# Optimization experiments

Hardware: AMD Instinct MI355X
Metric: run time of the kernel (lower is better)

## Reference

```python
import jax, jax.numpy as jnp
import numpy as np

D = 1024
B, S = 4, 2048


def setup_inputs() -> dict:
    key = jax.random.key(0)
    ks = jax.random.split(key, 9)
    std = 1.0 / np.sqrt(D)
    x = jax.random.normal(ks[0], (B, S, D), dtype=jnp.float32)
    Wq = jax.random.normal(ks[1], (D, D), dtype=jnp.float32) * std
    bq = jax.random.normal(ks[2], (D,), dtype=jnp.float32) * std
    Wk = jax.random.normal(ks[3], (D, D), dtype=jnp.float32) * std
    bk = jax.random.normal(ks[4], (D,), dtype=jnp.float32) * std
    Wv = jax.random.normal(ks[5], (D, D), dtype=jnp.float32) * std
    bv = jax.random.normal(ks[6], (D,), dtype=jnp.float32) * std
    Wo = jax.random.normal(ks[7], (D, D), dtype=jnp.float32) * std
    bo = jax.random.normal(ks[8], (D,), dtype=jnp.float32) * std
    return {"x": x, "Wq": Wq, "bq": bq, "Wk": Wk, "bk": bk,
            "Wv": Wv, "bv": bv, "Wo": Wo, "bo": bo}


def reference(x, Wq, bq, Wk, bk, Wv, bv, Wo, bo):
    d = x.shape[-1]
    q = x @ Wq + bq          # [B, S, D]
    k = x @ Wk + bk          # [B, S, D] (first call: kv cache empty)
    v = x @ Wv + bv          # [B, S, D]
    scale = 1.0 / jnp.sqrt(jnp.asarray(d, dtype=x.dtype))
    att = jnp.einsum('bqd,bkd->bqk', q, k) * scale  # [B, S, S]
    sq, sk = q.shape[1], k.shape[1]
    causal = jnp.triu(jnp.ones((sq, sk), dtype=bool), k=1)
    att = jnp.where(causal, -jnp.inf, att)
    att = jax.nn.softmax(att, axis=-1)
    out = jnp.einsum('bqk,bkd->bqd', att, v)        # [B, S, D]
    return out @ Wo + bo
```

## Files before the change

kernel.cpp:

```cpp
#include <hip/hip_runtime.h>
#include <hip/hip_bf16.h>


typedef __attribute__((ext_vector_type(8))) __bf16 bf16x8;
typedef __attribute__((ext_vector_type(4))) float f32x4;
typedef __attribute__((ext_vector_type(8))) unsigned short u16x8;
typedef __attribute__((ext_vector_type(4))) float float4v;
typedef long long ll;

static __device__ __forceinline__ unsigned short f2b(float f) {
  unsigned int u = __float_as_uint(f);
  u += 0x7fffu + ((u >> 16) & 1u);
  return (unsigned short)(u >> 16);
}
static __device__ __forceinline__ float b2f(unsigned short b) {
  return __uint_as_float(((unsigned int)b) << 16);
}

static __device__ __forceinline__ void gload16(const unsigned short* g, unsigned short* l) {
  __builtin_amdgcn_global_load_lds(
      (const __attribute__((address_space(1))) void*)g,
      (__attribute__((address_space(3))) void*)l, 16, 0, 0);
}

__global__ __launch_bounds__(256) void cvt_f32_bf16(const float* __restrict__ in,
                                                    unsigned short* __restrict__ out,
                                                    long long n) {
  long long i = ((long long)blockIdx.x * 256 + threadIdx.x) * 8;
  if (i + 8 > n) return;
  float4v a = *(const float4v*)(in + i);
  float4v b = *(const float4v*)(in + i + 4);
  u16x8 o;
  o[0] = f2b(a[0]); o[1] = f2b(a[1]); o[2] = f2b(a[2]); o[3] = f2b(a[3]);
  o[4] = f2b(b[0]); o[5] = f2b(b[1]); o[6] = f2b(b[2]); o[7] = f2b(b[3]);
  *(u16x8*)(out + i) = o;
}

__global__ __launch_bounds__(256) void transpose_cvt(const float* __restrict__ in,
                                                     unsigned short* __restrict__ out, int n) {
  __shared__ float t[32][33];
  int bx = blockIdx.x * 32, by = blockIdx.y * 32;
  int tx = threadIdx.x, ty = threadIdx.y;
#pragma unroll
  for (int i = 0; i < 32; i += 8)
    t[ty + i][tx] = in[(ll)(by + ty + i) * n + bx + tx];
  __syncthreads();
#pragma unroll
  for (int i = 0; i < 32; i += 8)
    out[(ll)(bx + ty + i) * n + by + tx] = f2b(t[tx][ty + i]);
}

__global__ void concat2(const float* __restrict__ a, const float* __restrict__ b,
                        float* __restrict__ o, int n) {
  int i = blockIdx.x * 256 + threadIdx.x;
  if (i < n) { o[i] = a[i]; o[i + n] = b[i]; }
}

template <int CAUSAL>
__global__ __launch_bounds__(256, 2) void gemm_tn(
    const unsigned short* __restrict__ A, const unsigned short* __restrict__ B,
    const float* __restrict__ bias, void* __restrict__ C,
    int K, int lda, int ldb, int ldc,
    ll strideA, ll strideB, ll strideC,
    float alpha, int c_is_bf16, int bias_row) {
  __shared__ unsigned short sA[2][128][64];
  __shared__ unsigned short sB[2][128][64];

  const int tid = threadIdx.x;
  const int w = tid >> 6, lane = tid & 63;
  const int bz = blockIdx.z;
  const unsigned short* Ab = A + (ll)bz * strideA;
  const unsigned short* Bb = B + (ll)bz * strideB;
  const int brow = blockIdx.y * 128, bcol = blockIdx.x * 128;
  const int wr = (w >> 1) * 64, wc = (w & 1) * 64;
  const int lr = lane & 15, lk = lane >> 4;

  const int Keff = (CAUSAL == 2) ? (brow + 128) : K;
  const int nt = Keff >> 6;

  f32x4 acc[4][4];
#pragma unroll
  for (int i = 0; i < 4; ++i)
#pragma unroll
    for (int n = 0; n < 4; ++n) acc[i][n] = (f32x4){0.f, 0.f, 0.f, 0.f};

  auto STAGE = [&](int buf, int kb) {
#pragma unroll
    for (int it = 0; it < 4; ++it) {
      const int chunk = it * 4 + w;
      const int slot = chunk * 64 + lane;
      const int row = slot >> 3;
      const int kg = (slot & 7) ^ (row & 7);
      gload16(Ab + (ll)(brow + row) * lda + kb + kg * 8, &sA[buf][0][0] + chunk * 512);
      gload16(Bb + (ll)(bcol + row) * ldb + kb + kg * 8, &sB[buf][0][0] + chunk * 512);
    }
  };

  auto COMPUTE = [&](int buf) {
#pragma unroll
    for (int kk = 0; kk < 64; kk += 32) {
      bf16x8 af[4], bfr[4];
      const int kgb = (kk >> 3) + lk;
      const int sw = (kgb ^ (lr & 7)) * 8;
#pragma unroll
      for (int i = 0; i < 4; ++i) af[i] = *(const bf16x8*)&sA[buf][wr + i * 16 + lr][sw];
#pragma unroll
      for (int n = 0; n < 4; ++n) bfr[n] = *(const bf16x8*)&sB[buf][wc + n * 16 + lr][sw];
#pragma unroll
      for (int i = 0; i < 4; ++i)
#pragma unroll
        for (int n = 0; n < 4; ++n)
          acc[i][n] = __builtin_amdgcn_mfma_f32_16x16x32_bf16(af[i], bfr[n], acc[i][n], 0, 0, 0);
    }
  };

  STAGE(0, 0);
  __syncthreads();
  int cur = 0;
  for (int t = 0; t < nt - 1; ++t) {
    STAGE(cur ^ 1, (t + 1) << 6);
    COMPUTE(cur);
    __syncthreads();
    cur ^= 1;
  }
  COMPUTE(cur);

  ll cbase = (ll)bz * strideC;
#pragma unroll
  for (int i = 0; i < 4; ++i) {
    int row = brow + wr + i * 16 + lk * 4;
#pragma unroll
    for (int n = 0; n < 4; ++n) {
      int col = bcol + wc + n * 16 + lr;
#pragma unroll
      for (int r = 0; r < 4; ++r) {
        float bvv = bias ? (bias_row ? bias[row + r] : bias[col]) : 0.0f;
        float v = (acc[i][n][r] + bvv) * alpha;
        ll idx = cbase + (ll)(row + r) * ldc + col;
        if (c_is_bf16) ((unsigned short*)C)[idx] = f2b(v);
        else ((float*)C)[idx] = v;
      }
    }
  }
}

template <int CAUSAL>
__global__ __launch_bounds__(512, 2) void gemm8p(
    const unsigned short* __restrict__ A, const unsigned short* __restrict__ B,
    const float* __restrict__ bias, void* __restrict__ C,
    int K, int lda, int ldb, int ldc,
    ll strideA, ll strideB, ll strideC,
    float alpha, int c_is_bf16) {
  if (CAUSAL == 1 && blockIdx.x > blockIdx.y) return;

  __shared__ unsigned short smem[4 * 16384];

  const int tid = threadIdx.x;
  const int wid = tid >> 6, lane = tid & 63;
  const int wm = wid >> 2, wn = wid & 3;
  const int lr = lane & 15, lk = lane >> 4;
  const int bz = blockIdx.z;
  const unsigned short* Ab = A + (ll)bz * strideA;
  const unsigned short* Bb = B + (ll)bz * strideB;
  const int brow = blockIdx.y * 256, bcol = blockIdx.x * 256;
  const int nt = K >> 5;

  f32x4 acc[8][4];
#pragma unroll
  for (int m = 0; m < 8; ++m)
#pragma unroll
    for (int n = 0; n < 4; ++n) acc[m][n] = (f32x4){0.f, 0.f, 0.f, 0.f};

  auto STAGE_A = [&](int t) {
    unsigned short* lds = &smem[0] + (t & 3) * 16384;
    const int kb = t << 5;
#pragma unroll
    for (int h = 0; h < 2; ++h) {
      const int c = wid * 2 + h;
      const int row = c * 16 + (lane >> 2);
      const int kg = (lane & 3) ^ ((row >> 1) & 3);
      gload16(Ab + (ll)(brow + row) * lda + kb + kg * 8, lds + c * 512);
    }
  };
  auto STAGE_B = [&](int t) {
    unsigned short* lds = &smem[0] + (t & 3) * 16384 + 8192;
    const int kb = t << 5;
#pragma unroll
    for (int h = 0; h < 2; ++h) {
      const int c = wid * 2 + h;
      const int row = c * 16 + (lane >> 2);
      const int kg = (lane & 3) ^ ((row >> 1) & 3);
      gload16(Bb + (ll)(bcol + row) * ldb + kb + kg * 8, lds + c * 512);
    }
  };

  STAGE_A(0); STAGE_B(0);
  STAGE_A(1); STAGE_B(1);

  for (int t = 0; t < nt; ++t) {
    if (t < nt - 1) asm volatile("s_waitcnt vmcnt(4)" ::: "memory");
    else            asm volatile("s_waitcnt vmcnt(0)" ::: "memory");
    __builtin_amdgcn_s_barrier();

    const unsigned short* lds = &smem[0] + (t & 3) * 16384;
    bf16x8 bfrag[4], afrag[4];

#pragma unroll
    for (int n = 0; n < 4; ++n) {
      const int row = wn * 64 + n * 16 + lr;
      const int slot = lk ^ ((row >> 1) & 3);
      bfrag[n] = *(const bf16x8*)(lds + 8192 + row * 32 + slot * 8);
    }
#pragma unroll
    for (int m = 0; m < 4; ++m) {
      const int row = wm * 128 + m * 16 + lr;
      const int slot = lk ^ ((row >> 1) & 3);
      afrag[m] = *(const bf16x8*)(lds + row * 32 + slot * 8);
    }
    if (t + 2 < nt) STAGE_A(t + 2);
    __builtin_amdgcn_s_barrier();
    __builtin_amdgcn_s_setprio(1);
#pragma unroll
    for (int m = 0; m < 4; ++m)
#pragma unroll
      for (int n = 0; n < 4; ++n)
        acc[m][n] = __builtin_amdgcn_mfma_f32_16x16x32_bf16(afrag[m], bfrag[n], acc[m][n], 0, 0, 0);
    __builtin_amdgcn_s_setprio(0);
    __builtin_amdgcn_s_barrier();

#pragma unroll
    for (int m = 0; m < 4; ++m) {
      const int row = wm * 128 + (m + 4) * 16 + lr;
      const int slot = lk ^ ((row >> 1) & 3);
      afrag[m] = *(const bf16x8*)(lds + row * 32 + slot * 8);
    }
    if (t + 2 < nt) STAGE_B(t + 2);
    __builtin_amdgcn_s_barrier();
    __builtin_amdgcn_s_setprio(1);
#pragma unroll
    for (int m = 0; m < 4; ++m)
#pragma unroll
      for (int n = 0; n < 4; ++n)
        acc[m + 4][n] = __builtin_amdgcn_mfma_f32_16x16x32_bf16(afrag[m], bfrag[n], acc[m + 4][n], 0, 0, 0);
    __builtin_amdgcn_s_setprio(0);
  }

  ll cbase = (ll)bz * strideC;
#pragma unroll
  for (int m = 0; m < 8; ++m) {
    const int row0 = brow + wm * 128 + m * 16 + lk * 4;
#pragma unroll
    for (int n = 0; n < 4; ++n) {
      const int col = bcol + wn * 64 + n * 16 + lr;
#pragma unroll
      for (int r = 0; r < 4; ++r) {
        float bvv = bias ? bias[col] : 0.0f;
        float v = (acc[m][n][r] + bvv) * alpha;
        ll idx = cbase + (ll)(row0 + r) * ldc + col;
        if (c_is_bf16) ((unsigned short*)C)[idx] = f2b(v);
        else ((float*)C)[idx] = v;
      }
    }
  }
}

__global__ __launch_bounds__(256) void softmax_row2048(unsigned short* __restrict__ S) {
  const int r = blockIdx.x, b = blockIdx.y;
  unsigned short* row = S + ((ll)b * 2048 + r) * 2048;
  const int tid = threadIdx.x;
  const int i0 = tid * 8;
  __shared__ float red[4];

  u16x8 v = *(const u16x8*)(row + i0);
  float f[8];
  float m = -3.0e38f;
#pragma unroll
  for (int j = 0; j < 8; ++j) {
    f[j] = (i0 + j <= r) ? b2f(v[j]) : -3.0e38f;
    m = fmaxf(m, f[j]);
  }
#pragma unroll
  for (int o = 1; o < 64; o <<= 1) m = fmaxf(m, __shfl_xor(m, o, 64));
  if ((tid & 63) == 0) red[tid >> 6] = m;
  __syncthreads();
  m = fmaxf(fmaxf(red[0], red[1]), fmaxf(red[2], red[3]));
  __syncthreads();

  float e[8];
  float s = 0.0f;
#pragma unroll
  for (int j = 0; j < 8; ++j) {
    e[j] = (i0 + j <= r) ? __expf(f[j] - m) : 0.0f;
    s += e[j];
  }
#pragma unroll
  for (int o = 1; o < 64; o <<= 1) s += __shfl_xor(s, o, 64);
  if ((tid & 63) == 0) red[tid >> 6] = s;
  __syncthreads();
  s = red[0] + red[1] + red[2] + red[3];
  float inv = 1.0f / s;
  u16x8 o8;
#pragma unroll
  for (int j = 0; j < 8; ++j) o8[j] = f2b(e[j] * inv);
  *(u16x8*)(row + i0) = o8;
}

extern "C" void kernel_launch(void* const* d_in, const int* in_sizes, int n_in,
                              void* d_out, int out_size, void* d_ws, size_t ws_size,
                              hipStream_t stream) {
  const float* x  = (const float*)d_in[0];
  const float* Wq = (const float*)d_in[1];
  const float* bq = (const float*)d_in[2];
  const float* Wk = (const float*)d_in[3];
  const float* bk = (const float*)d_in[4];
  const float* Wv = (const float*)d_in[5];
  const float* bv = (const float*)d_in[6];
  const float* Wo = (const float*)d_in[7];
  const float* bo = (const float*)d_in[8];

  const int B = 4, S = 2048, D = 1024;
  const ll MS = (ll)B * S;

  char* p = (char*)d_ws;
  unsigned short* xb   = (unsigned short*)p; p += MS * D * 2;
  unsigned short* Wqkt = (unsigned short*)p; p += (ll)2 * D * D * 2;
  unsigned short* Wvt  = (unsigned short*)p; p += (ll)D * D * 2;
  unsigned short* Wot  = (unsigned short*)p; p += (ll)D * D * 2;
  float*          bqkc = (float*)p;          p += 2 * D * 4;
  unsigned short* QKc  = (unsigned short*)p; p += MS * 2 * D * 2;
  unsigned short* Vt   = (unsigned short*)p; p += (ll)D * MS * 2;
  unsigned short* Sm   = (unsigned short*)p; p += (ll)B * S * S * 2;
  unsigned short* At   = (unsigned short*)p; p += MS * D * 2;

  dim3 blk(256);
  dim3 blk512(512);
  dim3 tblk(32, 8);

  cvt_f32_bf16<<<dim3(4096), blk, 0, stream>>>(x, xb, MS * D);
  transpose_cvt<<<dim3(32, 32), tblk, 0, stream>>>(Wq, Wqkt, D);
  transpose_cvt<<<dim3(32, 32), tblk, 0, stream>>>(Wk, Wqkt + (ll)D * D, D);
  transpose_cvt<<<dim3(32, 32), tblk, 0, stream>>>(Wv, Wvt, D);
  transpose_cvt<<<dim3(32, 32), tblk, 0, stream>>>(Wo, Wot, D);
  concat2<<<dim3(4), blk, 0, stream>>>(bq, bk, bqkc, D);

  gemm8p<0><<<dim3(8, 32, 1), blk512, 0, stream>>>(
      xb, Wqkt, bqkc, QKc, D, D, D, 2 * D, 0, 0, 0, 1.0f, 1);

  gemm_tn<0><<<dim3(64, 8, 1), blk, 0, stream>>>(
      Wvt, xb, bv, Vt, D, D, D, (int)MS, 0, 0, 0, 1.0f, 1, 1);

  gemm8p<1><<<dim3(8, 8, 4), blk512, 0, stream>>>(
      QKc, QKc + D, nullptr, Sm, D, 2 * D, 2 * D, S,
      (ll)S * 2 * D, (ll)S * 2 * D, (ll)S * S, 0.03125f, 1);

  softmax_row2048<<<dim3(S, B), blk, 0, stream>>>(Sm);

  gemm_tn<2><<<dim3(8, 16, 4), blk, 0, stream>>>(
      Sm, Vt, nullptr, At, S, S, (int)MS, D,
      (ll)S * S, (ll)S, (ll)S * D, 1.0f, 1, 0);

  gemm_tn<0><<<dim3(8, 64, 1), blk, 0, stream>>>(
      At, Wot, bo, d_out, D, D, D, D, 0, 0, 0, 1.0f, 0, 0);
}
```

Measured before the change: 340.7 us.

## Replace 128x128 double-buffered GEMM with 128x256 triple-buffered pipelined GEMM

Replaces the 256-thread 128x128 tile GEMM used for V projection, attention-times-V, and output projection with a 512-thread 128x256 tile kernel. The new kernel uses BK=32 and three LDS buffers with explicit vmcnt waits, interleaving staging of the next tiles between two MFMA halves under raised priority. The aim is better overlap of global loads with matrix math and more reuse per block. The trade-off is fewer blocks per launch, which may leave CUs underused on the smaller grids, and more barriers per K step.

```diff
diff --git a/kernel.cpp b/kernel.cpp
--- a/kernel.cpp
+++ b/kernel.cpp
@@ -57,94 +57,6 @@
 }
 
 template <int CAUSAL>
-__global__ __launch_bounds__(256, 2) void gemm_tn(
-    const unsigned short* __restrict__ A, const unsigned short* __restrict__ B,
-    const float* __restrict__ bias, void* __restrict__ C,
-    int K, int lda, int ldb, int ldc,
-    ll strideA, ll strideB, ll strideC,
-    float alpha, int c_is_bf16, int bias_row) {
-  __shared__ unsigned short sA[2][128][64];
-  __shared__ unsigned short sB[2][128][64];
-
-  const int tid = threadIdx.x;
-  const int w = tid >> 6, lane = tid & 63;
-  const int bz = blockIdx.z;
-  const unsigned short* Ab = A + (ll)bz * strideA;
-  const unsigned short* Bb = B + (ll)bz * strideB;
-  const int brow = blockIdx.y * 128, bcol = blockIdx.x * 128;
-  const int wr = (w >> 1) * 64, wc = (w & 1) * 64;
-  const int lr = lane & 15, lk = lane >> 4;
-
-  const int Keff = (CAUSAL == 2) ? (brow + 128) : K;
-  const int nt = Keff >> 6;
-
-  f32x4 acc[4][4];
-#pragma unroll
-  for (int i = 0; i < 4; ++i)
-#pragma unroll
-    for (int n = 0; n < 4; ++n) acc[i][n] = (f32x4){0.f, 0.f, 0.f, 0.f};
-
-  auto STAGE = [&](int buf, int kb) {
-#pragma unroll
-    for (int it = 0; it < 4; ++it) {
-      const int chunk = it * 4 + w;
-      const int slot = chunk * 64 + lane;
-      const int row = slot >> 3;
-      const int kg = (slot & 7) ^ (row & 7);
-      gload16(Ab + (ll)(brow + row) * lda + kb + kg * 8, &sA[buf][0][0] + chunk * 512);
-      gload16(Bb + (ll)(bcol + row) * ldb + kb + kg * 8, &sB[buf][0][0] + chunk * 512);
-    }
-  };
-
-  auto COMPUTE = [&](int buf) {
-#pragma unroll
-    for (int kk = 0; kk < 64; kk += 32) {
-      bf16x8 af[4], bfr[4];
-      const int kgb = (kk >> 3) + lk;
-      const int sw = (kgb ^ (lr & 7)) * 8;
-#pragma unroll
-      for (int i = 0; i < 4; ++i) af[i] = *(const bf16x8*)&sA[buf][wr + i * 16 + lr][sw];
-#pragma unroll
-      for (int n = 0; n < 4; ++n) bfr[n] = *(const bf16x8*)&sB[buf][wc + n * 16 + lr][sw];
-#pragma unroll
-      for (int i = 0; i < 4; ++i)
-#pragma unroll
-        for (int n = 0; n < 4; ++n)
-          acc[i][n] = __builtin_amdgcn_mfma_f32_16x16x32_bf16(af[i], bfr[n], acc[i][n], 0, 0, 0);
-    }
-  };
-
-  STAGE(0, 0);
-  __syncthreads();
-  int cur = 0;
-  for (int t = 0; t < nt - 1; ++t) {
-    STAGE(cur ^ 1, (t + 1) << 6);
-    COMPUTE(cur);
-    __syncthreads();
-    cur ^= 1;
-  }
-  COMPUTE(cur);
-
-  ll cbase = (ll)bz * strideC;
-#pragma unroll
-  for (int i = 0; i < 4; ++i) {
-    int row = brow + wr + i * 16 + lk * 4;
-#pragma unroll
-    for (int n = 0; n < 4; ++n) {
-      int col = bcol + wc + n * 16 + lr;
-#pragma unroll
-      for (int r = 0; r < 4; ++r) {
-        float bvv = bias ? (bias_row ? bias[row + r] : bias[col]) : 0.0f;
-        float v = (acc[i][n][r] + bvv) * alpha;
-        ll idx = cbase + (ll)(row + r) * ldc + col;
-        if (c_is_bf16) ((unsigned short*)C)[idx] = f2b(v);
-        else ((float*)C)[idx] = v;
-      }
-    }
-  }
-}
-
-template <int CAUSAL>
 __global__ __launch_bounds__(512, 2) void gemm8p(
     const unsigned short* __restrict__ A, const unsigned short* __restrict__ B,
     const float* __restrict__ bias, void* __restrict__ C,
@@ -255,6 +167,127 @@
 #pragma unroll
       for (int r = 0; r < 4; ++r) {
         float bvv = bias ? bias[col] : 0.0f;
+        float v = (acc[m][n][r] + bvv) * alpha;
+        ll idx = cbase + (ll)(row0 + r) * ldc + col;
+        if (c_is_bf16) ((unsigned short*)C)[idx] = f2b(v);
+        else ((float*)C)[idx] = v;
+      }
+    }
+  }
+}
+
+template <int CAUSAL>
+__global__ __launch_bounds__(512, 4) void gemmp(
+    const unsigned short* __restrict__ A, const unsigned short* __restrict__ B,
+    const float* __restrict__ bias, void* __restrict__ C,
+    int K, int lda, int ldb, int ldc,
+    ll strideA, ll strideB, ll strideC,
+    float alpha, int c_is_bf16, int bias_row) {
+  __shared__ unsigned short smem[3 * 12288];
+
+  const int tid = threadIdx.x;
+  const int wid = tid >> 6, lane = tid & 63;
+  const int wm = wid >> 2, wn = wid & 3;
+  const int lr = lane & 15, lk = lane >> 4;
+  const int bz = blockIdx.z;
+  const unsigned short* Ab = A + (ll)bz * strideA;
+  const unsigned short* Bb = B + (ll)bz * strideB;
+  const int brow = blockIdx.y * 128, bcol = blockIdx.x * 256;
+
+  const int Keff = (CAUSAL == 2) ? (brow + 128) : K;
+  const int nt = Keff >> 5;
+
+  f32x4 acc[4][4];
+#pragma unroll
+  for (int m = 0; m < 4; ++m)
+#pragma unroll
+    for (int n = 0; n < 4; ++n) acc[m][n] = (f32x4){0.f, 0.f, 0.f, 0.f};
+
+  auto STAGE_A = [&](int t, int b) {
+    unsigned short* lds = &smem[0] + b * 12288 + wid * 512;
+    const int kb = t << 5;
+    const int row = wid * 16 + (lane >> 2);
+    const int kg = (lane & 3) ^ ((row >> 1) & 3);
+    gload16(Ab + (ll)(brow + row) * lda + kb + kg * 8, lds);
+  };
+  auto STAGE_B = [&](int t, int b) {
+    unsigned short* lds0 = &smem[0] + b * 12288 + 4096;
+    const int kb = t << 5;
+#pragma unroll
+    for (int h = 0; h < 2; ++h) {
+      const int c = wid * 2 + h;
+      const int row = c * 16 + (lane >> 2);
+      const int kg = (lane & 3) ^ ((row >> 1) & 3);
+      gload16(Bb + (ll)(bcol + row) * ldb + kb + kg * 8, lds0 + c * 512);
+    }
+  };
+
+  STAGE_A(0, 0); STAGE_B(0, 0);
+  STAGE_A(1, 1); STAGE_B(1, 1);
+
+  int cur = 0;
+  for (int t = 0; t < nt; ++t) {
+    if (t < nt - 1) asm volatile("s_waitcnt vmcnt(3)" ::: "memory");
+    else            asm volatile("s_waitcnt vmcnt(0)" ::: "memory");
+    __builtin_amdgcn_s_barrier();
+
+    const unsigned short* ldsA = &smem[0] + cur * 12288;
+    const unsigned short* ldsB = ldsA + 4096;
+    int sbuf = cur + 2; if (sbuf >= 3) sbuf -= 3;
+    bf16x8 bfrag[4], afrag[4];
+
+#pragma unroll
+    for (int n = 0; n < 4; ++n) {
+      const int row = wn * 64 + n * 16 + lr;
+      const int slot = lk ^ ((row >> 1) & 3);
+      bfrag[n] = *(const bf16x8*)(ldsB + row * 32 + slot * 8);
+    }
+#pragma unroll
+    for (int m = 0; m < 2; ++m) {
+      const int row = wm * 64 + m * 16 + lr;
+      const int slot = lk ^ ((row >> 1) & 3);
+      afrag[m] = *(const bf16x8*)(ldsA + row * 32 + slot * 8);
+    }
+    if (t + 2 < nt) STAGE_A(t + 2, sbuf);
+    __builtin_amdgcn_s_barrier();
+    __builtin_amdgcn_s_setprio(1);
+#pragma unroll
+    for (int m = 0; m < 2; ++m)
+#pragma unroll
+      for (int n = 0; n < 4; ++n)
+        acc[m][n] = __builtin_amdgcn_mfma_f32_16x16x32_bf16(afrag[m], bfrag[n], acc[m][n], 0, 0, 0);
+    __builtin_amdgcn_s_setprio(0);
+    __builtin_amdgcn_s_barrier();
+
+#pragma unroll
+    for (int m = 2; m < 4; ++m) {
+      const int row = wm * 64 + m * 16 + lr;
+      const int slot = lk ^ ((row >> 1) & 3);
+      afrag[m] = *(const bf16x8*)(ldsA + row * 32 + slot * 8);
+    }
+    if (t + 2 < nt) STAGE_B(t + 2, sbuf);
+    __builtin_amdgcn_s_barrier();
+    __builtin_amdgcn_s_setprio(1);
+#pragma unroll
+    for (int m = 2; m < 4; ++m)
+#pragma unroll
+      for (int n = 0; n < 4; ++n)
+        acc[m][n] = __builtin_amdgcn_mfma_f32_16x16x32_bf16(afrag[m], bfrag[n], acc[m][n], 0, 0, 0);
+    __builtin_amdgcn_s_setprio(0);
+
+    cur = (cur == 2) ? 0 : cur + 1;
+  }
+
+  ll cbase = (ll)bz * strideC;
+#pragma unroll
+  for (int m = 0; m < 4; ++m) {
+    const int row0 = brow + wm * 64 + m * 16 + lk * 4;
+#pragma unroll
+    for (int n = 0; n < 4; ++n) {
+      const int col = bcol + wn * 64 + n * 16 + lr;
+#pragma unroll
+      for (int r = 0; r < 4; ++r) {
+        float bvv = bias ? (bias_row ? bias[row0 + r] : bias[col]) : 0.0f;
         float v = (acc[m][n][r] + bvv) * alpha;
         ll idx = cbase + (ll)(row0 + r) * ldc + col;
         if (c_is_bf16) ((unsigned short*)C)[idx] = f2b(v);
@@ -346,7 +379,7 @@
   gemm8p<0><<<dim3(8, 32, 1), blk512, 0, stream>>>(
       xb, Wqkt, bqkc, QKc, D, D, D, 2 * D, 0, 0, 0, 1.0f, 1);
 
-  gemm_tn<0><<<dim3(64, 8, 1), blk, 0, stream>>>(
+  gemmp<0><<<dim3(32, 8, 1), blk512, 0, stream>>>(
       Wvt, xb, bv, Vt, D, D, D, (int)MS, 0, 0, 0, 1.0f, 1, 1);
 
   gemm8p<1><<<dim3(8, 8, 4), blk512, 0, stream>>>(
@@ -355,10 +388,10 @@
 
   softmax_row2048<<<dim3(S, B), blk, 0, stream>>>(Sm);
 
-  gemm_tn<2><<<dim3(8, 16, 4), blk, 0, stream>>>(
+  gemmp<2><<<dim3(4, 16, 4), blk512, 0, stream>>>(
       Sm, Vt, nullptr, At, S, S, (int)MS, D,
       (ll)S * S, (ll)S, (ll)S * D, 1.0f, 1, 0);
 
-  gemm_tn<0><<<dim3(8, 64, 1), blk, 0, stream>>>(
+  gemmp<0><<<dim3(4, 64, 1), blk512, 0, stream>>>(
       At, Wot, bo, d_out, D, D, D, D, 0, 0, 0, 1.0f, 0, 0);
 }
```

Result: faster. 328.7 us (-3.5%).
